# Kernel optimization log

Hardware: AMD Instinct MI355X
Metric: run time of the kernel (lower is better)

Reference implementation:

```python
import jax, jax.numpy as jnp
import numpy as np

T, SEQ, IN, H, L, NC = 64, 128, 256, 512, 2, 10


def _xavier(key, shape):
    fan_out, fan_in = shape[0], shape[1]
    a = jnp.sqrt(6.0 / (fan_in + fan_out)).astype(jnp.float32)
    return jax.random.uniform(key, shape, jnp.float32, -a, a)


def setup_inputs() -> dict:
    key = jax.random.key(0)
    ks = jax.random.split(key, 16)
    inp = {"x": jax.random.normal(ks[0], (T, SEQ, IN), jnp.float32)}
    # LSTM layer 0 (input IN), layer 1 (input H). PyTorch gate order: i, f, g, o
    inp["w_ih0"] = _xavier(ks[1], (4 * H, IN))
    inp["w_hh0"] = _xavier(ks[2], (4 * H, H))
    inp["b_ih0"] = jnp.zeros((4 * H,), jnp.float32)
    inp["b_hh0"] = jnp.zeros((4 * H,), jnp.float32)
    inp["w_ih1"] = _xavier(ks[3], (4 * H, H))
    inp["w_hh1"] = _xavier(ks[4], (4 * H, H))
    inp["b_ih1"] = jnp.zeros((4 * H,), jnp.float32)
    inp["b_hh1"] = jnp.zeros((4 * H,), jnp.float32)
    # out_linear: Linear(SEQ*H, H) -> ReLU -> Linear(H, NC)
    inp["w1"] = _xavier(ks[5], (H, SEQ * H))
    inp["b1"] = jnp.zeros((H,), jnp.float32)
    inp["w2"] = _xavier(ks[6], (NC, H))
    inp["b2"] = jnp.zeros((NC,), jnp.float32)
    return inp


def _lstm_layer(x, w_ih, w_hh, b_ih, b_hh):
    # x: [T, B, I]; returns hidden sequence [T, B, H]
    B = x.shape[1]
    Hh = w_hh.shape[1]
    # precompute input-to-gate contributions for all timesteps
    xg = jnp.einsum('tbi,gi->tbg', x, w_ih) + b_ih  # [T, B, 4H]

    def step(carry, xg_t):
        h, c = carry
        g = xg_t + h @ w_hh.T + b_hh  # [B, 4H]
        i, f, gg, o = jnp.split(g, 4, axis=-1)
        i = jax.nn.sigmoid(i)
        f = jax.nn.sigmoid(f)
        gg = jnp.tanh(gg)
        o = jax.nn.sigmoid(o)
        c = f * c + i * gg
        h = o * jnp.tanh(c)
        return (h, c), h

    init = (jnp.zeros((B, Hh), x.dtype), jnp.zeros((B, Hh), x.dtype))
    _, ys = jax.lax.scan(step, init, xg)
    return ys


def reference(x, w_ih0, w_hh0, b_ih0, b_hh0, w_ih1, w_hh1, b_ih1, b_hh1, w1, b1, w2, b2):
    out = _lstm_layer(x, w_ih0, w_hh0, b_ih0, b_hh0)
    out = _lstm_layer(out, w_ih1, w_hh1, b_ih1, b_hh1)  # [T, SEQ, H]
    # dropout p=0.0 -> identity
    flat = out.reshape(out.shape[0], -1)  # [T, SEQ*H] (batched version of per-i loop)
    hmid = jax.nn.relu(flat @ w1.T + b1)
    return hmid @ w2.T + b2  # [T, NC]
```

## Files before the change

### kernel.cpp

```cpp
#include <hip/hip_runtime.h>

#define TT 64
#define BB 128
#define IND 256
#define HH 512
#define GG 2048
#define NCC 10
#define KFLAT 65536
#define HP2 520
#define SP 36

typedef __attribute__((ext_vector_type(8))) short bf16x8;
typedef __attribute__((ext_vector_type(4))) float floatx4;

__device__ __forceinline__ unsigned short f2bf(float x) {
    unsigned u = __builtin_bit_cast(unsigned, x);
    u += 0x7fffu + ((u >> 16) & 1u);
    return (unsigned short)(u >> 16);
}
__device__ __forceinline__ float bf2f(unsigned short h) {
    unsigned u = ((unsigned)h) << 16;
    return __builtin_bit_cast(float, u);
}
__device__ __forceinline__ float pk2f(unsigned u) {
    float hi = __builtin_bit_cast(float, u & 0xffff0000u);
    float lo = __builtin_bit_cast(float, u << 16);
    return hi + lo;
}

__global__ __launch_bounds__(256) void pack_split_kernel(
    const float* __restrict__ src, unsigned* __restrict__ dst, int n)
{
    for (int i = blockIdx.x * 256 + threadIdx.x; i < n; i += gridDim.x * 256) {
        float f = src[i];
        unsigned short hb = f2bf(f);
        unsigned short lb = f2bf(f - bf2f(hb));
        dst[i] = ((unsigned)hb << 16) | lb;
    }
}

__global__ __launch_bounds__(256) void gemm_pk_mfma(
    const unsigned* __restrict__ A, const unsigned* __restrict__ W,
    const float* __restrict__ b0, const float* __restrict__ b1,
    float* __restrict__ C, int K, int N)
{
    __shared__ short Ahi[128][SP], Alo[128][SP], Whi[128][SP], Wlo[128][SP];

    const int tid  = threadIdx.x;
    const int lane = tid & 63;
    const int wv   = tid >> 6;
    const int wm   = (wv & 1) * 64;
    const int wn   = (wv >> 1) * 64;
    const int l15  = lane & 15;
    const int quad = lane >> 4;
    const int m0   = blockIdx.x * 128;
    const int n0   = blockIdx.y * 128;

    floatx4 acc[4][4];
    #pragma unroll
    for (int i = 0; i < 4; ++i)
        #pragma unroll
        for (int j = 0; j < 4; ++j)
            acc[i][j] = (floatx4){0.f, 0.f, 0.f, 0.f};

    for (int kc = 0; kc < K; kc += 32) {
        #pragma unroll
        for (int it = 0; it < 4; ++it) {
            const int lin = it * 256 + tid;
            const int row = lin >> 3;
            const int c4  = (lin & 7) * 4;
            uint4 va = *(const uint4*)&A[(size_t)(m0 + row) * K + kc + c4];
            uint2 ah, al;
            ah.x = (va.x >> 16) | (va.y & 0xffff0000u);
            ah.y = (va.z >> 16) | (va.w & 0xffff0000u);
            al.x = (va.x & 0xffffu) | (va.y << 16);
            al.y = (va.z & 0xffffu) | (va.w << 16);
            *(uint2*)&Ahi[row][c4] = ah;
            *(uint2*)&Alo[row][c4] = al;
            uint4 vw = *(const uint4*)&W[(size_t)(n0 + row) * K + kc + c4];
            uint2 wh, wl;
            wh.x = (vw.x >> 16) | (vw.y & 0xffff0000u);
            wh.y = (vw.z >> 16) | (vw.w & 0xffff0000u);
            wl.x = (vw.x & 0xffffu) | (vw.y << 16);
            wl.y = (vw.z & 0xffffu) | (vw.w << 16);
            *(uint2*)&Whi[row][c4] = wh;
            *(uint2*)&Wlo[row][c4] = wl;
        }
        __syncthreads();

        bf16x8 afh[4], afl[4], bfh[4], bfl[4];
        #pragma unroll
        for (int i = 0; i < 4; ++i) {
            afh[i] = *(const bf16x8*)&Ahi[wm + i * 16 + l15][quad * 8];
            afl[i] = *(const bf16x8*)&Alo[wm + i * 16 + l15][quad * 8];
            bfh[i] = *(const bf16x8*)&Whi[wn + i * 16 + l15][quad * 8];
            bfl[i] = *(const bf16x8*)&Wlo[wn + i * 16 + l15][quad * 8];
        }
        #pragma unroll
        for (int i = 0; i < 4; ++i)
            #pragma unroll
            for (int j = 0; j < 4; ++j) {
                acc[i][j] = __builtin_amdgcn_mfma_f32_16x16x32_bf16(afh[i], bfh[j], acc[i][j], 0, 0, 0);
                acc[i][j] = __builtin_amdgcn_mfma_f32_16x16x32_bf16(afh[i], bfl[j], acc[i][j], 0, 0, 0);
                acc[i][j] = __builtin_amdgcn_mfma_f32_16x16x32_bf16(afl[i], bfh[j], acc[i][j], 0, 0, 0);
            }
        __syncthreads();
    }

    #pragma unroll
    for (int i = 0; i < 4; ++i) {
        #pragma unroll
        for (int j = 0; j < 4; ++j) {
            const int n = n0 + wn + j * 16 + l15;
            const float bias = b0[n] + b1[n];
            #pragma unroll
            for (int r = 0; r < 4; ++r) {
                const int m = m0 + wm + i * 16 + quad * 4 + r;
                C[(size_t)m * N + n] = acc[i][j][r] + bias;
            }
        }
    }
}

__device__ __forceinline__ unsigned stage8_atomic(
    const unsigned long long* __restrict__ src, int bb, int kk, unsigned exp,
    short (*Hs_hi)[HP2], short (*Hs_lo)[HP2])
{
    unsigned long long q0 = __hip_atomic_load(src + 0, __ATOMIC_RELAXED, __HIP_MEMORY_SCOPE_AGENT);
    unsigned long long q1 = __hip_atomic_load(src + 1, __ATOMIC_RELAXED, __HIP_MEMORY_SCOPE_AGENT);
    unsigned long long q2 = __hip_atomic_load(src + 2, __ATOMIC_RELAXED, __HIP_MEMORY_SCOPE_AGENT);
    unsigned long long q3 = __hip_atomic_load(src + 3, __ATOMIC_RELAXED, __HIP_MEMORY_SCOPE_AGENT);
    unsigned c0 = (unsigned)q0, c1 = (unsigned)(q0 >> 32);
    unsigned c2 = (unsigned)q1, c3 = (unsigned)(q1 >> 32);
    unsigned c4 = (unsigned)q2, c5 = (unsigned)(q2 >> 32);
    unsigned c6 = (unsigned)q3, c7 = (unsigned)(q3 >> 32);
    unsigned bad = ((c0 ^ exp) | (c1 ^ exp) | (c2 ^ exp) | (c3 ^ exp)
                  | (c4 ^ exp) | (c5 ^ exp) | (c6 ^ exp) | (c7 ^ exp)) & 0xFu;
    uint4 hiv, lov;
    hiv.x = (c0 >> 16) | (c1 & 0xffff0000u);
    hiv.y = (c2 >> 16) | (c3 & 0xffff0000u);
    hiv.z = (c4 >> 16) | (c5 & 0xffff0000u);
    hiv.w = (c6 >> 16) | (c7 & 0xffff0000u);
    lov.x = (c0 & 0xFFF0u) | ((c1 & 0xFFF0u) << 16);
    lov.y = (c2 & 0xFFF0u) | ((c3 & 0xFFF0u) << 16);
    lov.z = (c4 & 0xFFF0u) | ((c5 & 0xFFF0u) << 16);
    lov.w = (c6 & 0xFFF0u) | ((c7 & 0xFFF0u) << 16);
    *(uint4*)&Hs_hi[bb][kk] = hiv;
    *(uint4*)&Hs_lo[bb][kk] = lov;
    return bad;
}

__device__ __forceinline__ unsigned stage8_plain(
    const unsigned* __restrict__ src, int bb, int kk, unsigned exp,
    short (*Hs_hi)[HP2], short (*Hs_lo)[HP2])
{
    const uint4 v0 = *(const uint4*)(src);
    const uint4 v1 = *(const uint4*)(src + 4);
    unsigned bad = ((v0.x ^ exp) | (v0.y ^ exp) | (v0.z ^ exp) | (v0.w ^ exp)
                  | (v1.x ^ exp) | (v1.y ^ exp) | (v1.z ^ exp) | (v1.w ^ exp)) & 0xFu;
    uint4 hiv, lov;
    hiv.x = (v0.x >> 16) | (v0.y & 0xffff0000u);
    hiv.y = (v0.z >> 16) | (v0.w & 0xffff0000u);
    hiv.z = (v1.x >> 16) | (v1.y & 0xffff0000u);
    hiv.w = (v1.z >> 16) | (v1.w & 0xffff0000u);
    lov.x = (v0.x & 0xFFF0u) | ((v0.y & 0xFFF0u) << 16);
    lov.y = (v0.z & 0xFFF0u) | ((v0.w & 0xFFF0u) << 16);
    lov.z = (v1.x & 0xFFF0u) | ((v1.y & 0xFFF0u) << 16);
    lov.w = (v1.z & 0xFFF0u) | ((v1.w & 0xFFF0u) << 16);
    *(uint4*)&Hs_hi[bb][kk] = hiv;
    *(uint4*)&Hs_lo[bb][kk] = lov;
    return bad;
}

__device__ __forceinline__ void stage_tile_g(
    const unsigned* __restrict__ base, unsigned exp,
    int tstart, int pcount, int pstride,
    short (*Hs_hi)[HP2], short (*Hs_lo)[HP2])
{
    unsigned miss = 0;
    for (int p = 0; p < pcount; ++p) {
        const int idx = p * pstride + tstart;
        unsigned bad = stage8_plain(base + idx, idx >> 9, idx & 511,
                                    exp, Hs_hi, Hs_lo);
        miss |= (bad ? 1u : 0u) << p;
    }
    while (miss) {
        for (int p = 0; p < pcount; ++p) {
            if (miss & (1u << p)) {
                const int idx = p * pstride + tstart;
                if (!stage8_atomic((const unsigned long long*)(base + idx),
                                   idx >> 9, idx & 511, exp, Hs_hi, Hs_lo))
                    miss &= ~(1u << p);
            }
        }
    }
}

__device__ __forceinline__ void spin_cnt(const unsigned* p) {
    int n = 0;
    while (__hip_atomic_load(p, __ATOMIC_RELAXED, __HIP_MEMORY_SCOPE_AGENT) < 4u) {
        if (++n > 65536) break;
    }
}

__global__ __launch_bounds__(512, 2) void lstm_fused(
    const float* __restrict__ xg,
    const float* __restrict__ w_hh0,
    const float* __restrict__ w_ih1,
    const float* __restrict__ w_hh1,
    const float* __restrict__ b_ih1, const float* __restrict__ b_hh1,
    unsigned* __restrict__ hpack0,
    unsigned* __restrict__ hpack1,
    unsigned* __restrict__ flags)
{
    __shared__ short Ra_hi[32][HP2], Ra_lo[32][HP2];
    __shared__ short Xa_hi[32][HP2], Xa_lo[32][HP2];
    __shared__ float GsR[64][33];
    __shared__ float GsX[64][33];

    const int tid  = threadIdx.x;
    const int lane = tid & 63;
    const int wv   = tid >> 6;
    const bool isR = wv < 4;
    const int gate = wv & 3;
    const bool isB = blockIdx.x >= 128;
    const int blk  = blockIdx.x & 127;
    const int bt   = blk & 3;
    const int jsl  = blk >> 2;
    const int j0   = jsl * 16;
    const int l15  = lane & 15;
    const int quad = lane >> 4;
    const int tid_x = tid - 256;

    bf16x8 wf_hi[16], wf_lo[16];
    {
        const float* wsrc = isR ? (isB ? w_hh1 : w_hh0) : w_ih1;
        if (isR || isB) {
            const float* wrow = wsrc + (size_t)(gate * HH + j0 + l15) * HH + quad * 8;
            #pragma unroll
            for (int kc = 0; kc < 16; ++kc) {
                float f[8];
                *(float4*)&f[0] = *(const float4*)&wrow[kc * 32];
                *(float4*)&f[4] = *(const float4*)&wrow[kc * 32 + 4];
                bf16x8 vh, vl;
                #pragma unroll
                for (int j = 0; j < 8; ++j) {
                    unsigned short hb = f2bf(f[j]);
                    vh[j] = (short)hb;
                    vl[j] = (short)f2bf(f[j] - bf2f(hb));
                }
                wf_hi[kc] = vh; wf_lo[kc] = vl;
            }
        }
    }

    const int ju  = (tid & 7) * 2;
    const int bu2 = (tid >> 3) & 31;
    float bi0=0.f,bi1=0.f,bf0_=0.f,bf1_=0.f,bg0=0.f,bg1=0.f,bo0=0.f,bo1=0.f;
    if (isB && isR) {
        bi0 = b_ih1[j0+ju]        + b_hh1[j0+ju];
        bi1 = b_ih1[j0+ju+1]      + b_hh1[j0+ju+1];
        bf0_= b_ih1[HH+j0+ju]     + b_hh1[HH+j0+ju];
        bf1_= b_ih1[HH+j0+ju+1]   + b_hh1[HH+j0+ju+1];
        bg0 = b_ih1[2*HH+j0+ju]   + b_hh1[2*HH+j0+ju];
        bg1 = b_ih1[2*HH+j0+ju+1] + b_hh1[2*HH+j0+ju+1];
        bo0 = b_ih1[3*HH+j0+ju]   + b_hh1[3*HH+j0+ju];
        bo1 = b_ih1[3*HH+j0+ju+1] + b_hh1[3*HH+j0+ju+1];
    }

    for (int i = tid; i < 64 * 33; i += 512)
        ((float*)GsX)[i] = 0.f;
    __syncthreads();

    unsigned* hp_rec = isB ? hpack1 : hpack0;
    const int layerBase = isB ? 65 : 0;
    float c0 = 0.f, c1 = 0.f;

    for (int t = 0; t < TT; ++t) {
        const unsigned* rec_base = hp_rec + (size_t)t * (BB * HH) + (size_t)bt * 32 * HH;
        const unsigned* inp_base = hpack0 + (size_t)(t + 1) * (BB * HH) + (size_t)bt * 32 * HH;
        const unsigned expR = (unsigned)t % 9u;
        const unsigned expX = (unsigned)(t + 1) % 9u;
        const unsigned* cR = flags + ((layerBase + t) * 4 + bt) * 32;
        const unsigned* cX = flags + ((t + 1) * 4 + bt) * 32;

        float2 xgv[4];
        if (!isB && isR) {
            const float* base = xg + (size_t)t * (BB * GG)
                              + (size_t)(bt * 32 + bu2) * GG + j0 + ju;
            #pragma unroll
            for (int g = 0; g < 4; ++g)
                xgv[g] = *(const float2*)&base[g * HH];
        }

        if (wv == 0 && lane < 32 && t > 0) spin_cnt(cR + lane);
        if (isB && wv == 4 && lane < 32) spin_cnt(cX + lane);
        __syncthreads();

        if (isB) {
            if (isR) stage_tile_g(rec_base, expR, tid * 8,   8, 2048, Ra_hi, Ra_lo);
            else     stage_tile_g(inp_base, expX, tid_x * 8, 8, 2048, Xa_hi, Xa_lo);
        } else {
            stage_tile_g(rec_base, expR, tid * 8, 4, 4096, Ra_hi, Ra_lo);
        }
        __syncthreads();

        if (isR) {
            floatx4 a0 = {0.f,0.f,0.f,0.f}, a1 = {0.f,0.f,0.f,0.f};
            #pragma unroll
            for (int kc = 0; kc < 16; ++kc) {
                const int off = kc * 32 + quad * 8;
                bf16x8 r0h = *(const bf16x8*)&Ra_hi[l15][off];
                bf16x8 r0l = *(const bf16x8*)&Ra_lo[l15][off];
                bf16x8 r1h = *(const bf16x8*)&Ra_hi[16 + l15][off];
                bf16x8 r1l = *(const bf16x8*)&Ra_lo[16 + l15][off];
                a0 = __builtin_amdgcn_mfma_f32_16x16x32_bf16(wf_hi[kc], r0h, a0, 0, 0, 0);
                a1 = __builtin_amdgcn_mfma_f32_16x16x32_bf16(wf_hi[kc], r1h, a1, 0, 0, 0);
                a0 = __builtin_amdgcn_mfma_f32_16x16x32_bf16(wf_hi[kc], r0l, a0, 0, 0, 0);
                a1 = __builtin_amdgcn_mfma_f32_16x16x32_bf16(wf_hi[kc], r1l, a1, 0, 0, 0);
                a0 = __builtin_amdgcn_mfma_f32_16x16x32_bf16(wf_lo[kc], r0h, a0, 0, 0, 0);
                a1 = __builtin_amdgcn_mfma_f32_16x16x32_bf16(wf_lo[kc], r1h, a1, 0, 0, 0);
            }
            #pragma unroll
            for (int r = 0; r < 4; ++r) {
                GsR[gate * 16 + quad * 4 + r][l15]      = a0[r];
                GsR[gate * 16 + quad * 4 + r][16 + l15] = a1[r];
            }
        } else if (isB) {
            floatx4 a0 = {0.f,0.f,0.f,0.f}, a1 = {0.f,0.f,0.f,0.f};
            #pragma unroll
            for (int kc = 0; kc < 16; ++kc) {
                const int off = kc * 32 + quad * 8;
                bf16x8 x0h = *(const bf16x8*)&Xa_hi[l15][off];
                bf16x8 x0l = *(const bf16x8*)&Xa_lo[l15][off];
                bf16x8 x1h = *(const bf16x8*)&Xa_hi[16 + l15][off];
                bf16x8 x1l = *(const bf16x8*)&Xa_lo[16 + l15][off];
                a0 = __builtin_amdgcn_mfma_f32_16x16x32_bf16(wf_hi[kc], x0h, a0, 0, 0, 0);
                a1 = __builtin_amdgcn_mfma_f32_16x16x32_bf16(wf_hi[kc], x1h, a1, 0, 0, 0);
                a0 = __builtin_amdgcn_mfma_f32_16x16x32_bf16(wf_hi[kc], x0l, a0, 0, 0, 0);
                a1 = __builtin_amdgcn_mfma_f32_16x16x32_bf16(wf_hi[kc], x1l, a1, 0, 0, 0);
                a0 = __builtin_amdgcn_mfma_f32_16x16x32_bf16(wf_lo[kc], x0h, a0, 0, 0, 0);
                a1 = __builtin_amdgcn_mfma_f32_16x16x32_bf16(wf_lo[kc], x1h, a1, 0, 0, 0);
            }
            #pragma unroll
            for (int r = 0; r < 4; ++r) {
                GsX[gate * 16 + quad * 4 + r][l15]      = a0[r];
                GsX[gate * 16 + quad * 4 + r][16 + l15] = a1[r];
            }
        }
        __syncthreads();

        if (isR) {
            const unsigned tag = (unsigned)(t + 1) % 9u;
            float gi0 = GsR[ju][bu2]      + GsX[ju][bu2];
            float gi1 = GsR[ju+1][bu2]    + GsX[ju+1][bu2];
            float gf0 = GsR[16+ju][bu2]   + GsX[16+ju][bu2];
            float gf1 = GsR[17+ju][bu2]   + GsX[17+ju][bu2];
            float gg0 = GsR[32+ju][bu2]   + GsX[32+ju][bu2];
            float gg1 = GsR[33+ju][bu2]   + GsX[33+ju][bu2];
            float go0 = GsR[48+ju][bu2]   + GsX[48+ju][bu2];
            float go1 = GsR[49+ju][bu2]   + GsX[49+ju][bu2];
            if (isB) {
                gi0 += bi0; gi1 += bi1; gf0 += bf0_; gf1 += bf1_;
                gg0 += bg0; gg1 += bg1; go0 += bo0; go1 += bo1;
            } else {
                gi0 += xgv[0].x; gi1 += xgv[0].y;
                gf0 += xgv[1].x; gf1 += xgv[1].y;
                gg0 += xgv[2].x; gg1 += xgv[2].y;
                go0 += xgv[3].x; go1 += xgv[3].y;
            }
            const float si0 = 1.f / (1.f + __expf(-gi0));
            const float sf0 = 1.f / (1.f + __expf(-gf0));
            const float tg0 = 2.f / (1.f + __expf(-2.f * gg0)) - 1.f;
            const float so0 = 1.f / (1.f + __expf(-go0));
            c0 = sf0 * c0 + si0 * tg0;
            const float th0 = 2.f / (1.f + __expf(-2.f * c0)) - 1.f;
            const float h0v = so0 * th0;
            const float si1 = 1.f / (1.f + __expf(-gi1));
            const float sf1 = 1.f / (1.f + __expf(-gf1));
            const float tg1 = 2.f / (1.f + __expf(-2.f * gg1)) - 1.f;
            const float so1 = 1.f / (1.f + __expf(-go1));
            c1 = sf1 * c1 + si1 * tg1;
            const float th1 = 2.f / (1.f + __expf(-2.f * c1)) - 1.f;
            const float h1v = so1 * th1;
            const unsigned short hb0 = f2bf(h0v);
            const unsigned short lb0 = f2bf(h0v - bf2f(hb0));
            const unsigned short hb1 = f2bf(h1v);
            const unsigned short lb1 = f2bf(h1v - bf2f(hb1));
            const unsigned pk0 = ((unsigned)hb0 << 16) | ((unsigned)lb0 & 0xFFF0u) | tag;
            const unsigned pk1 = ((unsigned)hb1 << 16) | ((unsigned)lb1 & 0xFFF0u) | tag;
            const unsigned long long pk64 =
                (unsigned long long)pk0 | ((unsigned long long)pk1 << 32);
            __hip_atomic_store(
                (unsigned long long*)&hp_rec[(size_t)(t + 1) * (BB * HH)
                    + (size_t)(bt * 32 + bu2) * HH + j0 + ju],
                pk64, __ATOMIC_RELAXED, __HIP_MEMORY_SCOPE_AGENT);

            asm volatile("s_waitcnt vmcnt(0)" ::: "memory");
            if (lane == 0)
                __hip_atomic_fetch_add(
                    (unsigned*)(flags + ((layerBase + (t + 1)) * 4 + bt) * 32 + jsl),
                    1u, __ATOMIC_RELAXED, __HIP_MEMORY_SCOPE_AGENT);
        }
    }
}

__global__ __launch_bounds__(256) void cls_partial_kernel(
    const unsigned* __restrict__ A, const float* __restrict__ W,
    float* __restrict__ part)
{
    const int n0 = blockIdx.x * 64;
    const int s  = blockIdx.y;
    const int kbase = s * 2048;
    const int tid = threadIdx.x;
    __shared__ float As[32][68];
    __shared__ float Bs[32][68];
    const int tm = tid >> 4, tn = tid & 15;
    float acc[4][4] = {};

    for (int kt = 0; kt < 2048; kt += 32) {
        #pragma unroll
        for (int q = tid; q < 512; q += 256) {
            const int mm = q >> 3;
            const int kq = q & 7;
            uint4 v = *(const uint4*)&A[(size_t)mm * KFLAT + kbase + kt + kq * 4];
            As[kq*4+0][mm] = pk2f(v.x & 0xFFFFFFF0u); As[kq*4+1][mm] = pk2f(v.y & 0xFFFFFFF0u);
            As[kq*4+2][mm] = pk2f(v.z & 0xFFFFFFF0u); As[kq*4+3][mm] = pk2f(v.w & 0xFFFFFFF0u);
            float4 w = *(const float4*)&W[(size_t)(n0 + mm) * KFLAT + kbase + kt + kq * 4];
            Bs[kq*4+0][mm] = w.x; Bs[kq*4+1][mm] = w.y;
            Bs[kq*4+2][mm] = w.z; Bs[kq*4+3][mm] = w.w;
        }
        __syncthreads();
        #pragma unroll
        for (int k = 0; k < 32; ++k) {
            float4 a = *(const float4*)&As[k][tm * 4];
            float4 b = *(const float4*)&Bs[k][tn * 4];
            acc[0][0] += a.x*b.x; acc[0][1] += a.x*b.y; acc[0][2] += a.x*b.z; acc[0][3] += a.x*b.w;
            acc[1][0] += a.y*b.x; acc[1][1] += a.y*b.y; acc[1][2] += a.y*b.z; acc[1][3] += a.y*b.w;
            acc[2][0] += a.z*b.x; acc[2][1] += a.z*b.y; acc[2][2] += a.z*b.z; acc[2][3] += a.z*b.w;
            acc[3][0] += a.w*b.x; acc[3][1] += a.w*b.y; acc[3][2] += a.w*b.z; acc[3][3] += a.w*b.w;
        }
        __syncthreads();
    }
    #pragma unroll
    for (int i = 0; i < 4; ++i) {
        const int m = tm * 4 + i;
        #pragma unroll
        for (int j = 0; j < 4; ++j) {
            part[((size_t)s * 64 + m) * 512 + n0 + tn * 4 + j] = acc[i][j];
        }
    }
}

__global__ __launch_bounds__(256) void cls_final_kernel(
    const float* __restrict__ part, const float* __restrict__ b1,
    const float* __restrict__ w2, const float* __restrict__ b2,
    float* __restrict__ out)
{
    const int t = blockIdx.x;
    __shared__ float hm[512];
    for (int n = threadIdx.x; n < 512; n += 256) {
        float sacc = b1[n];
        for (int sl = 0; sl < 32; ++sl)
            sacc += part[((size_t)sl * 64 + t) * 512 + n];
        hm[n] = fmaxf(sacc, 0.f);
    }
    __syncthreads();
    if (threadIdx.x < NCC) {
        float sacc = b2[threadIdx.x];
        const float* wr = w2 + (size_t)threadIdx.x * 512;
        for (int n = 0; n < 512; ++n) sacc += hm[n] * wr[n];
        out[t * NCC + threadIdx.x] = sacc;
    }
}

extern "C" void kernel_launch(void* const* d_in, const int* in_sizes, int n_in,
                              void* d_out, int out_size, void* d_ws, size_t ws_size,
                              hipStream_t stream)
{
    const float* x     = (const float*)d_in[0];
    const float* w_ih0 = (const float*)d_in[1];
    const float* w_hh0 = (const float*)d_in[2];
    const float* b_ih0 = (const float*)d_in[3];
    const float* b_hh0 = (const float*)d_in[4];
    const float* w_ih1 = (const float*)d_in[5];
    const float* w_hh1 = (const float*)d_in[6];
    const float* b_ih1 = (const float*)d_in[7];
    const float* b_hh1 = (const float*)d_in[8];
    const float* w1    = (const float*)d_in[9];
    const float* b1    = (const float*)d_in[10];
    const float* w2    = (const float*)d_in[11];
    const float* b2    = (const float*)d_in[12];
    float* out = (float*)d_out;

    float*    ws     = (float*)d_ws;
    float*    xg     = ws;
    unsigned* hpack0 = (unsigned*)(xg + (size_t)8192 * 2048);
    unsigned* hpack1 = hpack0 + (size_t)65 * BB * HH;
    unsigned* xpk    = hpack1;
    unsigned* w0pk   = xpk + (size_t)8192 * IND;
    float*    part   = (float*)(hpack1 + (size_t)65 * BB * HH);
    unsigned* flags  = (unsigned*)part;

    pack_split_kernel<<<1024, 256, 0, stream>>>(x, xpk, 8192 * IND);
    pack_split_kernel<<<512,  256, 0, stream>>>(w_ih0, w0pk, GG * IND);
    hipMemsetAsync(hpack0, 0, (size_t)BB * HH * sizeof(unsigned), stream);
    hipMemsetAsync(flags, 0, (size_t)2 * 65 * 4 * 32 * sizeof(unsigned), stream);

    gemm_pk_mfma<<<dim3(8192 / 128, GG / 128), 256, 0, stream>>>(
        xpk, w0pk, b_ih0, b_hh0, xg, IND, GG);

    hipMemsetAsync(hpack1, 0, (size_t)BB * HH * sizeof(unsigned), stream);

    lstm_fused<<<256, 512, 0, stream>>>(
        xg, w_hh0, w_ih1, w_hh1, b_ih1, b_hh1, hpack0, hpack1, flags);

    cls_partial_kernel<<<dim3(512 / 64, 32), 256, 0, stream>>>(
        hpack1 + (size_t)BB * HH, w1, part);
    cls_final_kernel<<<64, 256, 0, stream>>>(part, b1, w2, b2, out);
}
```

Baseline: 860.3 us.

## Read recurrent state from small ring buffer and use per-block ready flags

The recurrent hidden state is now also written to a 4-slot ring buffer, and readers stage from it first, falling back to the full history buffer when the tag check fails. The per-wave counter increments with a vmcnt wait become one flag store per block after a barrier, and the spin-wait checks for a nonzero flag and skips the block's own slot. Block indices are also remapped so each group of 8 consecutive blocks holds both layers and all batch tiles of one hidden slice. The aim is to cut cross-block synchronisation latency and keep the recurrent reads in a cache-resident region. In exchange it adds an extra store per step and relies on the tag check to catch stale ring slots.

```diff
diff --git a/kernel.cpp b/kernel.cpp
--- a/kernel.cpp
+++ b/kernel.cpp
@@ -172,33 +172,41 @@
     return bad;
 }
 
+__device__ __forceinline__ void stage_tile_fs(
+    const unsigned* __restrict__ fastb, const unsigned* __restrict__ safeb,
+    unsigned exp, int tstart, int pcount, int pstride,
+    short (*Hs_hi)[HP2], short (*Hs_lo)[HP2])
+{
+    unsigned miss = 0;
+    for (int p = 0; p < pcount; ++p) {
+        const int idx = p * pstride + tstart;
+        unsigned bad = stage8_plain(fastb + idx, idx >> 9, idx & 511,
+                                    exp, Hs_hi, Hs_lo);
+        miss |= (bad ? 1u : 0u) << p;
+    }
+    while (miss) {
+        for (int p = 0; p < pcount; ++p) {
+            if (miss & (1u << p)) {
+                const int idx = p * pstride + tstart;
+                if (!stage8_atomic((const unsigned long long*)(safeb + idx),
+                                   idx >> 9, idx & 511, exp, Hs_hi, Hs_lo))
+                    miss &= ~(1u << p);
+            }
+        }
+    }
+}
+
 __device__ __forceinline__ void stage_tile_g(
     const unsigned* __restrict__ base, unsigned exp,
     int tstart, int pcount, int pstride,
     short (*Hs_hi)[HP2], short (*Hs_lo)[HP2])
 {
-    unsigned miss = 0;
-    for (int p = 0; p < pcount; ++p) {
-        const int idx = p * pstride + tstart;
-        unsigned bad = stage8_plain(base + idx, idx >> 9, idx & 511,
-                                    exp, Hs_hi, Hs_lo);
-        miss |= (bad ? 1u : 0u) << p;
-    }
-    while (miss) {
-        for (int p = 0; p < pcount; ++p) {
-            if (miss & (1u << p)) {
-                const int idx = p * pstride + tstart;
-                if (!stage8_atomic((const unsigned long long*)(base + idx),
-                                   idx >> 9, idx & 511, exp, Hs_hi, Hs_lo))
-                    miss &= ~(1u << p);
-            }
-        }
-    }
-}
-
-__device__ __forceinline__ void spin_cnt(const unsigned* p) {
+    stage_tile_fs(base, base, exp, tstart, pcount, pstride, Hs_hi, Hs_lo);
+}
+
+__device__ __forceinline__ void spin_flag(const unsigned* p) {
     int n = 0;
-    while (__hip_atomic_load(p, __ATOMIC_RELAXED, __HIP_MEMORY_SCOPE_AGENT) < 4u) {
+    while (__hip_atomic_load(p, __ATOMIC_RELAXED, __HIP_MEMORY_SCOPE_AGENT) == 0u) {
         if (++n > 65536) break;
     }
 }
@@ -211,6 +219,8 @@
     const float* __restrict__ b_ih1, const float* __restrict__ b_hh1,
     unsigned* __restrict__ hpack0,
     unsigned* __restrict__ hpack1,
+    unsigned* __restrict__ ring0,
+    unsigned* __restrict__ ring1,
     unsigned* __restrict__ flags)
 {
     __shared__ short Ra_hi[32][HP2], Ra_lo[32][HP2];
@@ -223,10 +233,10 @@
     const int wv   = tid >> 6;
     const bool isR = wv < 4;
     const int gate = wv & 3;
-    const bool isB = blockIdx.x >= 128;
-    const int blk  = blockIdx.x & 127;
-    const int bt   = blk & 3;
-    const int jsl  = blk >> 2;
+    const int c8   = blockIdx.x & 7;
+    const bool isB = (c8 >> 2) != 0;
+    const int bt   = c8 & 3;
+    const int jsl  = blockIdx.x >> 3;
     const int j0   = jsl * 16;
     const int l15  = lane & 15;
     const int quad = lane >> 4;
@@ -272,17 +282,19 @@
         ((float*)GsX)[i] = 0.f;
     __syncthreads();
 
-    unsigned* hp_rec = isB ? hpack1 : hpack0;
+    unsigned* hp_safe = isB ? hpack1 : hpack0;
+    unsigned* ring    = isB ? ring1  : ring0;
     const int layerBase = isB ? 65 : 0;
     float c0 = 0.f, c1 = 0.f;
 
     for (int t = 0; t < TT; ++t) {
-        const unsigned* rec_base = hp_rec + (size_t)t * (BB * HH) + (size_t)bt * 32 * HH;
+        const unsigned* rec_fast = ring + (size_t)(t & 3) * (BB * HH) + (size_t)bt * 32 * HH;
+        const unsigned* rec_safe = hp_safe + (size_t)t * (BB * HH) + (size_t)bt * 32 * HH;
         const unsigned* inp_base = hpack0 + (size_t)(t + 1) * (BB * HH) + (size_t)bt * 32 * HH;
         const unsigned expR = (unsigned)t % 9u;
         const unsigned expX = (unsigned)(t + 1) % 9u;
-        const unsigned* cR = flags + ((layerBase + t) * 4 + bt) * 32;
-        const unsigned* cX = flags + ((t + 1) * 4 + bt) * 32;
+        const unsigned* fR = flags + ((layerBase + t) * 4 + bt) * 32;
+        const unsigned* fX = flags + ((t + 1) * 4 + bt) * 32;
 
         float2 xgv[4];
         if (!isB && isR) {
@@ -293,15 +305,15 @@
                 xgv[g] = *(const float2*)&base[g * HH];
         }
 
-        if (wv == 0 && lane < 32 && t > 0) spin_cnt(cR + lane);
-        if (isB && wv == 4 && lane < 32) spin_cnt(cX + lane);
+        if (wv == 0 && lane < 32 && t > 0 && lane != jsl) spin_flag(fR + lane);
+        if (isB && wv == 4 && lane < 32) spin_flag(fX + lane);
         __syncthreads();
 
         if (isB) {
-            if (isR) stage_tile_g(rec_base, expR, tid * 8,   8, 2048, Ra_hi, Ra_lo);
-            else     stage_tile_g(inp_base, expX, tid_x * 8, 8, 2048, Xa_hi, Xa_lo);
+            if (isR) stage_tile_fs(rec_fast, rec_safe, expR, tid * 8,   8, 2048, Ra_hi, Ra_lo);
+            else     stage_tile_g (inp_base,           expX, tid_x * 8, 8, 2048, Xa_hi, Xa_lo);
         } else {
-            stage_tile_g(rec_base, expR, tid * 8, 4, 4096, Ra_hi, Ra_lo);
+            stage_tile_fs(rec_fast, rec_safe, expR, tid * 8, 4, 4096, Ra_hi, Ra_lo);
         }
         __syncthreads();
 
@@ -391,17 +403,18 @@
             const unsigned pk1 = ((unsigned)hb1 << 16) | ((unsigned)lb1 & 0xFFF0u) | tag;
             const unsigned long long pk64 =
                 (unsigned long long)pk0 | ((unsigned long long)pk1 << 32);
+            const size_t cell = (size_t)(bt * 32 + bu2) * HH + j0 + ju;
+            *(unsigned long long*)&ring[(size_t)((t + 1) & 3) * (BB * HH) + cell] = pk64;
             __hip_atomic_store(
-                (unsigned long long*)&hp_rec[(size_t)(t + 1) * (BB * HH)
-                    + (size_t)(bt * 32 + bu2) * HH + j0 + ju],
+                (unsigned long long*)&hp_safe[(size_t)(t + 1) * (BB * HH) + cell],
                 pk64, __ATOMIC_RELAXED, __HIP_MEMORY_SCOPE_AGENT);
-
-            asm volatile("s_waitcnt vmcnt(0)" ::: "memory");
-            if (lane == 0)
-                __hip_atomic_fetch_add(
-                    (unsigned*)(flags + ((layerBase + (t + 1)) * 4 + bt) * 32 + jsl),
-                    1u, __ATOMIC_RELAXED, __HIP_MEMORY_SCOPE_AGENT);
-        }
+        }
+        __syncthreads();
+
+        if (tid == 0)
+            __hip_atomic_store(
+                flags + ((layerBase + (t + 1)) * 4 + bt) * 32 + jsl,
+                1u, __ATOMIC_RELAXED, __HIP_MEMORY_SCOPE_AGENT);
     }
 }
 
@@ -501,11 +514,15 @@
     unsigned* w0pk   = xpk + (size_t)8192 * IND;
     float*    part   = (float*)(hpack1 + (size_t)65 * BB * HH);
     unsigned* flags  = (unsigned*)part;
+    unsigned* ring0  = (unsigned*)((char*)part + (1 << 20));
+    unsigned* ring1  = (unsigned*)((char*)part + (2 << 20));
 
     pack_split_kernel<<<1024, 256, 0, stream>>>(x, xpk, 8192 * IND);
     pack_split_kernel<<<512,  256, 0, stream>>>(w_ih0, w0pk, GG * IND);
     hipMemsetAsync(hpack0, 0, (size_t)BB * HH * sizeof(unsigned), stream);
     hipMemsetAsync(flags, 0, (size_t)2 * 65 * 4 * 32 * sizeof(unsigned), stream);
+    hipMemsetAsync(ring0, 0, (size_t)BB * HH * sizeof(unsigned), stream);
+    hipMemsetAsync(ring1, 0, (size_t)BB * HH * sizeof(unsigned), stream);
 
     gemm_pk_mfma<<<dim3(8192 / 128, GG / 128), 256, 0, stream>>>(
         xpk, w0pk, b_ih0, b_hh0, xg, IND, GG);
@@ -513,7 +530,7 @@
     hipMemsetAsync(hpack1, 0, (size_t)BB * HH * sizeof(unsigned), stream);
 
     lstm_fused<<<256, 512, 0, stream>>>(
-        xg, w_hh0, w_ih1, w_hh1, b_ih1, b_hh1, hpack0, hpack1, flags);
+        xg, w_hh0, w_ih1, w_hh1, b_ih1, b_hh1, hpack0, hpack1, ring0, ring1, flags);
 
     cls_partial_kernel<<<dim3(512 / 64, 32), 256, 0, stream>>>(
         hpack1 + (size_t)BB * HH, w1, part);
```

Measured after the change: 854.1 us. About the same (-0.7%).
